# Kernel tuning notes

Measured on AMD Instinct MI355X. Metric: run time of the kernel, lower is better.

Reference implementation:

```python
import jax, jax.numpy as jnp
import numpy as np

S, E, H, D, F = 2048, 1280, 16, 80, 5120
EPS = 1e-6


def _ln(x, g, b):
    m = x.mean(-1, keepdims=True)
    v = x.var(-1, keepdims=True)
    return (x - m) * jax.lax.rsqrt(v + EPS) * g + b


def _rotate_half(x):
    x1, x2 = jnp.split(x, 2, axis=-1)
    return jnp.concatenate([-x2, x1], axis=-1)


def _quick_gelu(x):
    return x * jax.nn.sigmoid(1.702 * x)


def setup_inputs() -> dict:
    key = jax.random.key(0)
    ks = jax.random.split(key, 12)
    inp = {
        "hidden_states": jax.random.normal(ks[0], (S, E), jnp.float32),
        "attention_mask": jnp.ones((1, 1, S, S), jnp.bool_),
        "cos": jax.random.uniform(ks[1], (S, D), jnp.float32),
        "sin": jax.random.uniform(ks[2], (S, D), jnp.float32),
        "ln1_g": jnp.ones((E,), jnp.float32),
        "ln1_b": jnp.zeros((E,), jnp.float32),
        "ln2_g": jnp.ones((E,), jnp.float32),
        "ln2_b": jnp.zeros((E,), jnp.float32),
        "w_qkv": jax.random.normal(ks[3], (E, 3 * E), jnp.float32) * (E ** -0.5),
        "b_qkv": jax.random.normal(ks[4], (3 * E,), jnp.float32) * 0.02,
        "w_o": jax.random.normal(ks[5], (E, E), jnp.float32) * (E ** -0.5),
        "b_o": jax.random.normal(ks[6], (E,), jnp.float32) * 0.02,
        "w_fc1": jax.random.normal(ks[7], (E, F), jnp.float32) * (E ** -0.5),
        "b_fc1": jax.random.normal(ks[8], (F,), jnp.float32) * 0.02,
        "w_fc2": jax.random.normal(ks[9], (F, E), jnp.float32) * (F ** -0.5),
        "b_fc2": jax.random.normal(ks[10], (E,), jnp.float32) * 0.02,
    }
    return inp


def reference(hidden_states, attention_mask, cos, sin, ln1_g, ln1_b, ln2_g, ln2_b,
              w_qkv, b_qkv, w_o, b_o, w_fc1, b_fc1, w_fc2, b_fc2):
    x = hidden_states  # [S, E]
    h = _ln(x, ln1_g, ln1_b)
    qkv = h @ w_qkv + b_qkv  # [S, 3E]
    q, k, v = jnp.split(qkv, 3, axis=-1)
    q = q.reshape(S, H, D)
    k = k.reshape(S, H, D)
    v = v.reshape(S, H, D)
    # rotary in fp32, cos/sin broadcast over head axis: [S, 1, D]
    c = cos[:, None, :].astype(jnp.float32)
    s = sin[:, None, :].astype(jnp.float32)
    qf, kf = q.astype(jnp.float32), k.astype(jnp.float32)
    q = (qf * c + _rotate_half(qf) * s).astype(q.dtype)
    k = (kf * c + _rotate_half(kf) * s).astype(k.dtype)
    # attention scores [H, S, S]
    scores = jnp.einsum('shd,thd->hst', q, k) / np.float32(np.sqrt(D))
    scores = jnp.where(attention_mask[0], scores, jnp.finfo(scores.dtype).min)
    probs = jax.nn.softmax(scores.astype(jnp.float32), axis=-1).astype(q.dtype)
    attn = jnp.einsum('hst,thd->shd', probs, v).reshape(S, E)
    attn = attn @ w_o + b_o
    x = x + attn
    h2 = _ln(x, ln2_g, ln2_b)
    mlp = _quick_gelu(h2 @ w_fc1 + b_fc1) @ w_fc2 + b_fc2
    return x + mlp
```

## Files before the change

### kernel.cpp

```cpp
#include <hip/hip_runtime.h>
#include <stdint.h>
#include <math.h>

#define S_LEN 2048
#define EMB   1280
#define NHEAD 16
#define HDIM  80
#define FDIM  5120

typedef __bf16 bf16x8 __attribute__((ext_vector_type(8)));
typedef float  f32x4  __attribute__((ext_vector_type(4)));
typedef int    i32x4  __attribute__((ext_vector_type(4)));
typedef unsigned short u16x8 __attribute__((ext_vector_type(8)));
typedef unsigned short u16x4 __attribute__((ext_vector_type(4)));

__device__ __forceinline__ float b2f(unsigned short u) {
    union { float f; unsigned int i; } x; x.i = ((unsigned int)u) << 16; return x.f;
}
__device__ __forceinline__ unsigned short f2b(float f) {
    union { float f; unsigned int i; } x; x.f = f;
    unsigned int r = x.i + 0x7FFFu + ((x.i >> 16) & 1u);
    return (unsigned short)(r >> 16);
}

__device__ __forceinline__ float wave_rsum(float v) {
    #pragma unroll
    for (int o = 32; o; o >>= 1) v += __shfl_down(v, o);
    return v;
}

__device__ __forceinline__ void trans64(
    const float* __restrict__ in, unsigned short* __restrict__ out,
    int R, int C, int bx, int by, int tid)
{
    __shared__ unsigned short tile[64][65];
    int c0 = bx * 64, r0 = by * 64;
    int tx = tid & 63, ty = tid >> 6;
    #pragma unroll
    for (int j = 0; j < 16; ++j) {
        int row = ty + j * 4;
        tile[row][tx] = f2b(in[(size_t)(r0 + row) * C + c0 + tx]);
    }
    __syncthreads();
    #pragma unroll
    for (int j = 0; j < 16; ++j) {
        int row = ty + j * 4;
        out[(size_t)(c0 + row) * R + r0 + tx] = tile[tx][row];
    }
}

__global__ __launch_bounds__(256) void transpose4_kernel(
    const float* __restrict__ w_qkv, unsigned short* __restrict__ wT_qkv,
    const float* __restrict__ w_o,   unsigned short* __restrict__ wT_o,
    const float* __restrict__ w_fc1, unsigned short* __restrict__ wT_fc1,
    const float* __restrict__ w_fc2, unsigned short* __restrict__ wT_fc2)
{
    int id = blockIdx.x, tid = threadIdx.x;
    if (id < 1200) {
        trans64(w_qkv, wT_qkv, 1280, 3840, id % 60, id / 60, tid);
    } else if (id < 1600) {
        int t = id - 1200;
        trans64(w_o, wT_o, 1280, 1280, t % 20, t / 20, tid);
    } else if (id < 3200) {
        int t = id - 1600;
        trans64(w_fc1, wT_fc1, 1280, 5120, t % 80, t / 80, tid);
    } else {
        int t = id - 3200;
        trans64(w_fc2, wT_fc2, 5120, 1280, t % 20, t / 20, tid);
    }
}

__global__ __launch_bounds__(256) void ln_kernel(
    const float* __restrict__ x,
    const float* __restrict__ g,
    const float* __restrict__ b,
    unsigned short* __restrict__ out)
{
    int row = blockIdx.x, tid = threadIdx.x;
    int lane = tid & 63, wave = tid >> 6;
    const float* xr = x + (size_t)row * EMB;
    float v[5], s = 0.f, ss = 0.f;
    #pragma unroll
    for (int i = 0; i < 5; ++i) {
        float f = xr[tid + i * 256];
        v[i] = f; s += f; ss += f * f;
    }
    s = wave_rsum(s); ss = wave_rsum(ss);
    __shared__ float rs[4], rss[4];
    if (lane == 0) { rs[wave] = s; rss[wave] = ss; }
    __syncthreads();
    float st  = rs[0] + rs[1] + rs[2] + rs[3];
    float sst = rss[0] + rss[1] + rss[2] + rss[3];
    float mean = st * (1.0f / EMB);
    float var  = sst * (1.0f / EMB) - mean * mean;
    float inv  = rsqrtf(var + 1e-6f);
    unsigned short* orow = out + (size_t)row * EMB;
    #pragma unroll
    for (int i = 0; i < 5; ++i) {
        int c = tid + i * 256;
        orow[c] = f2b((v[i] - mean) * inv * g[c] + b[c]);
    }
}

template<int EPI, int OM, int SPLIT>
__global__ __launch_bounds__(256) void gemm_kernel(
    const unsigned short* __restrict__ A,
    const unsigned short* __restrict__ Bt,
    const float* __restrict__ bias,
    const float* __restrict__ res,
    void* __restrict__ Cv,
    int M, int N, int K)
{
    __shared__ __align__(16) unsigned short As[2][128 * 32];
    __shared__ __align__(16) unsigned short Bs[2][128 * 32];

    int tid = threadIdx.x;
    int lane = tid & 63, wave = tid >> 6;
    int m0 = blockIdx.x * 128, n0 = blockIdx.y * 128;
    int wm = (wave >> 1) * 64, wn = (wave & 1) * 64;
    int kc = K / SPLIT;
    int kbeg = blockIdx.z * kc;
    const int NITER = kc / 32;

    f32x4 acc[4][4];
    #pragma unroll
    for (int i = 0; i < 4; ++i)
        #pragma unroll
        for (int j = 0; j < 4; ++j)
            acc[i][j] = (f32x4){0.f, 0.f, 0.f, 0.f};

    const unsigned short* Ap0 = A  + (size_t)(m0 + (tid >> 2)) * K + (tid & 3) * 8 + kbeg;
    const unsigned short* Ap1 = Ap0 + (size_t)64 * K;
    const unsigned short* Bp0 = Bt + (size_t)(n0 + (tid >> 2)) * K + (tid & 3) * 8 + kbeg;
    const unsigned short* Bp1 = Bp0 + (size_t)64 * K;

    int arow = lane & 15, aq = (lane >> 4) * 8;
    int aoff[4], boff[4];
    #pragma unroll
    for (int i = 0; i < 4; ++i) {
        aoff[i] = (wm + i * 16 + arow) * 32 + aq;
        boff[i] = (wn + i * 16 + arow) * 32 + aq;
    }

    i32x4 rA0a, rA1a, rB0a, rB1a, rA0b, rA1b, rB0b, rB1b;

    rA0b = *(const i32x4*)(Ap0);
    rA1b = *(const i32x4*)(Ap1);
    rB0b = *(const i32x4*)(Bp0);
    rB1b = *(const i32x4*)(Bp1);
    *(i32x4*)&As[0][tid * 8]        = rA0b;
    *(i32x4*)&As[0][2048 + tid * 8] = rA1b;
    *(i32x4*)&Bs[0][tid * 8]        = rB0b;
    *(i32x4*)&Bs[0][2048 + tid * 8] = rB1b;
    if (NITER > 1) {
        rA0a = *(const i32x4*)(Ap0 + 32);
        rA1a = *(const i32x4*)(Ap1 + 32);
        rB0a = *(const i32x4*)(Bp0 + 32);
        rB1a = *(const i32x4*)(Bp1 + 32);
    }
    __syncthreads();

#define GSTEP(IT, AW0, AW1, BW0, BW1, AL0, AL1, BL0, BL1)                    \
    {                                                                         \
        const int cur = (IT) & 1, nb = cur ^ 1;                               \
        if ((IT) + 1 < NITER) {                                               \
            *(i32x4*)&As[nb][tid * 8]        = AW0;                           \
            *(i32x4*)&As[nb][2048 + tid * 8] = AW1;                           \
            *(i32x4*)&Bs[nb][tid * 8]        = BW0;                           \
            *(i32x4*)&Bs[nb][2048 + tid * 8] = BW1;                           \
        }                                                                     \
        if ((IT) + 2 < NITER) {                                               \
            int ko = ((IT) + 2) * 32;                                         \
            AL0 = *(const i32x4*)(Ap0 + ko);                                  \
            AL1 = *(const i32x4*)(Ap1 + ko);                                  \
            BL0 = *(const i32x4*)(Bp0 + ko);                                  \
            BL1 = *(const i32x4*)(Bp1 + ko);                                  \
        }                                                                     \
        bf16x8 af[4], bfm[4];                                                 \
        _Pragma("unroll") for (int i = 0; i < 4; ++i) {                       \
            af[i]  = *(const bf16x8*)&As[cur][aoff[i]];                       \
            bfm[i] = *(const bf16x8*)&Bs[cur][boff[i]];                       \
        }                                                                     \
        _Pragma("unroll") for (int mi = 0; mi < 4; ++mi)                      \
            _Pragma("unroll") for (int ni = 0; ni < 4; ++ni)                  \
                acc[mi][ni] = __builtin_amdgcn_mfma_f32_16x16x32_bf16(        \
                    af[mi], bfm[ni], acc[mi][ni], 0, 0, 0);                   \
        __syncthreads();                                                      \
    }

    for (int it = 0; it < NITER; it += 2) {
        GSTEP(it,     rA0a, rA1a, rB0a, rB1a, rA0b, rA1b, rB0b, rB1b)
        GSTEP(it + 1, rA0b, rA1b, rB0b, rB1b, rA0a, rA1a, rB0a, rB1a)
    }
#undef GSTEP

    int col = lane & 15;
    int rbase = (lane >> 4) * 4;
    #pragma unroll
    for (int ni = 0; ni < 4; ++ni) {
        int gn = n0 + wn + ni * 16 + col;
        float bv = (OM == 2) ? 0.f : bias[gn];
        #pragma unroll
        for (int mi = 0; mi < 4; ++mi) {
            int gm = m0 + wm + mi * 16 + rbase;
            #pragma unroll
            for (int r = 0; r < 4; ++r) {
                float v = acc[mi][ni][r] + bv;
                if (OM != 2) {
                    if (EPI == 1) v = v / (1.0f + expf(-1.702f * v));
                }
                if (OM == 2)
                    ((float*)Cv)[((size_t)blockIdx.z * M + gm + r) * N + gn] = v;
                else if (OM == 1)
                    ((float*)Cv)[(size_t)(gm + r) * N + gn] = v;
                else
                    ((unsigned short*)Cv)[(size_t)(gm + r) * N + gn] = f2b(v);
            }
        }
    }
}

template<int Z>
__global__ __launch_bounds__(256) void reduceZ_kernel(
    const float* __restrict__ part,
    const float* __restrict__ res,
    const float* __restrict__ bias,
    float* __restrict__ out)
{
    size_t i4 = ((size_t)blockIdx.x * 256 + threadIdx.x) * 4;
    int colb = (int)(i4 % EMB);
    f32x4 a = *(const f32x4*)&res[i4];
    f32x4 bv = *(const f32x4*)&bias[colb];
    a += bv;
    const size_t slice = (size_t)S_LEN * EMB;
    #pragma unroll
    for (int z = 0; z < Z; ++z)
        a += *(const f32x4*)&part[z * slice + i4];
    *(f32x4*)&out[i4] = a;
}

__global__ __launch_bounds__(256) void ropev_kernel(
    const unsigned short* __restrict__ qkv,
    const float* __restrict__ cosb,
    const float* __restrict__ sinb,
    unsigned short* __restrict__ q_out,
    unsigned short* __restrict__ k_out,
    unsigned short* __restrict__ vt)
{
    __shared__ unsigned short qT[64 * 84];
    __shared__ unsigned short kT[64 * 84];
    __shared__ unsigned short vT[64 * 84];

    int h = blockIdx.x >> 5, stile = blockIdx.x & 31;
    int s0 = stile * 64;
    int tid = threadIdx.x;

    u16x4 qr[5], kr[5];
    #pragma unroll
    for (int i = 0; i < 5; ++i) {
        int u = tid + i * 256;
        int row = u / 20, col = (u % 20) * 4;
        const unsigned short* base = qkv + (size_t)(s0 + row) * (3 * EMB) + h * HDIM + col;
        qr[i] = *(const u16x4*)base;
        kr[i] = *(const u16x4*)(base + EMB);
        u16x4 v4 = *(const u16x4*)(base + 2 * EMB);
        *(u16x4*)&qT[row * 84 + col] = qr[i];
        *(u16x4*)&kT[row * 84 + col] = kr[i];
        *(u16x4*)&vT[row * 84 + col] = v4;
    }
    __syncthreads();

    #pragma unroll
    for (int i = 0; i < 5; ++i) {
        int u = tid + i * 256;
        int row = u / 20, col = (u % 20) * 4;
        int pcol = (col < 40) ? col + 40 : col - 40;
        float sgn = (col < 40) ? -1.f : 1.f;
        u16x4 qp = *(const u16x4*)&qT[row * 84 + pcol];
        u16x4 kp = *(const u16x4*)&kT[row * 84 + pcol];
        f32x4 c4 = *(const f32x4*)&cosb[(size_t)(s0 + row) * HDIM + col];
        f32x4 s4 = *(const f32x4*)&sinb[(size_t)(s0 + row) * HDIM + col];
        u16x4 qo, ko;
        #pragma unroll
        for (int j = 0; j < 4; ++j) {
            qo[j] = f2b(b2f(qr[i][j]) * c4[j] + sgn * b2f(qp[j]) * s4[j]);
            ko[j] = f2b(b2f(kr[i][j]) * c4[j] + sgn * b2f(kp[j]) * s4[j]);
        }
        size_t o = ((size_t)h * S_LEN + s0 + row) * HDIM + col;
        *(u16x4*)&q_out[o] = qo;
        *(u16x4*)&k_out[o] = ko;
    }
    #pragma unroll
    for (int i = 0; i < 5; ++i) {
        int w = tid + i * 256;
        int d = w >> 4, c4i = (w & 15) * 4;
        u16x4 pk;
        #pragma unroll
        for (int j = 0; j < 4; ++j) pk[j] = vT[(c4i + j) * 84 + d];
        *(u16x4*)(vt + ((size_t)h * HDIM + d) * S_LEN + s0 + c4i) = pk;
    }
}

__global__ __launch_bounds__(256) void fattn_kernel(
    const unsigned short* __restrict__ q,
    const unsigned short* __restrict__ k,
    const unsigned short* __restrict__ vt,
    unsigned short* __restrict__ out)
{
    __shared__ __align__(16) unsigned short Ks[2][64 * 96];
    __shared__ __align__(16) unsigned short Vs[2][80 * 72];
    __shared__ __align__(16) unsigned short Pt[4 * 16 * 72];

    int tid = threadIdx.x;
    int lane = tid & 63, wave = tid >> 6;
    int arow = lane & 15, quad = lane >> 4;
    int h = blockIdx.x >> 5, qb = blockIdx.x & 31;
    int s0 = qb * 64;
    const float c = 0.16129856f;

    const unsigned short* kbase = k + (size_t)h * S_LEN * HDIM;
    const unsigned short* vbase = vt + (size_t)h * HDIM * S_LEN;

    bf16x8 qf[3];
    {
        const unsigned short* qrp =
            q + ((size_t)h * S_LEN + s0 + wave * 16 + arow) * HDIM;
        #pragma unroll
        for (int kk = 0; kk < 3; ++kk) {
            int col = kk * 32 + quad * 8;
            u16x8 qv = (u16x8){0, 0, 0, 0, 0, 0, 0, 0};
            if (col < HDIM) qv = *(const u16x8*)(qrp + col);
            u16x8 qs8;
            #pragma unroll
            for (int j = 0; j < 8; ++j) qs8[j] = f2b(b2f(qv[j]) * c);
            qf[kk] = *(bf16x8*)&qs8;
        }
    }

    {
        int zr = tid >> 2, zc = 80 + (tid & 3) * 4;
        int zidx = (zr * 96 + zc) ^ ((zr & 7) << 3);
        *(u16x4*)&Ks[0][zidx] = (u16x4){0, 0, 0, 0};
        *(u16x4*)&Ks[1][zidx] = (u16x4){0, 0, 0, 0};
    }

    u16x4 kreg[5], vreg[5];
    #pragma unroll
    for (int i = 0; i < 5; ++i) {
        int u = tid + i * 256;
        kreg[i] = *(const u16x4*)(kbase + u * 4);
        vreg[i] = *(const u16x4*)(vbase + (size_t)(u >> 4) * S_LEN + (u & 15) * 4);
    }
    #pragma unroll
    for (int i = 0; i < 5; ++i) {
        int u = tid + i * 256;
        int row = u / 20, c4 = (u % 20) * 4;
        *(u16x4*)&Ks[0][(row * 96 + c4) ^ ((row & 7) << 3)] = kreg[i];
        *(u16x4*)&Vs[0][(u >> 4) * 72 + (u & 15) * 4] = vreg[i];
    }
    #pragma unroll
    for (int i = 0; i < 5; ++i) {
        int u = tid + i * 256;
        kreg[i] = *(const u16x4*)(kbase + (size_t)64 * HDIM + u * 4);
        vreg[i] = *(const u16x4*)(vbase + (size_t)(u >> 4) * S_LEN + 64 + (u & 15) * 4);
    }
    __syncthreads();

    int ksw[3];
    #pragma unroll
    for (int kk = 0; kk < 3; ++kk)
        ksw[kk] = (arow * 96 + kk * 32 + quad * 8) ^ ((arow & 7) << 3);

    int pw = wave * 16 * 72;
    float l_part = 0.f;
    f32x4 o[5];
    #pragma unroll
    for (int di = 0; di < 5; ++di) o[di] = (f32x4){0.f, 0.f, 0.f, 0.f};

    const int NIT = S_LEN / 64;
    for (int it = 0; it < NIT; ++it) {
        int cur = it & 1;
        if (it + 1 < NIT) {
            int nb = (it + 1) & 1;
            #pragma unroll
            for (int i = 0; i < 5; ++i) {
                int u = tid + i * 256;
                int row = u / 20, c4 = (u % 20) * 4;
                *(u16x4*)&Ks[nb][(row * 96 + c4) ^ ((row & 7) << 3)] = kreg[i];
                *(u16x4*)&Vs[nb][(u >> 4) * 72 + (u & 15) * 4] = vreg[i];
            }
        }
        if (it + 2 < NIT) {
            int t0 = (it + 2) * 64;
            #pragma unroll
            for (int i = 0; i < 5; ++i) {
                int u = tid + i * 256;
                kreg[i] = *(const u16x4*)(kbase + (size_t)t0 * HDIM + u * 4);
                vreg[i] = *(const u16x4*)(vbase + (size_t)(u >> 4) * S_LEN + t0 + (u & 15) * 4);
            }
        }

        f32x4 sc[4];
        #pragma unroll
        for (int ni = 0; ni < 4; ++ni) sc[ni] = (f32x4){0.f, 0.f, 0.f, 0.f};
        __builtin_amdgcn_s_setprio(1);
        #pragma unroll
        for (int kk = 0; kk < 3; ++kk) {
            bf16x8 bq = qf[kk];
            #pragma unroll
            for (int ni = 0; ni < 4; ++ni) {
                bf16x8 ak = *(const bf16x8*)&Ks[cur][ksw[kk] + ni * 1536];
                sc[ni] = __builtin_amdgcn_mfma_f32_16x16x32_bf16(ak, bq, sc[ni], 0, 0, 0);
            }
        }
        __builtin_amdgcn_s_setprio(0);

        #pragma unroll
        for (int ni = 0; ni < 4; ++ni) {
            u16x4 pk;
            #pragma unroll
            for (int r = 0; r < 4; ++r) {
                float p = __builtin_amdgcn_exp2f(sc[ni][r]);
                l_part += p;
                __bf16 pb = (__bf16)p;
                pk[r] = *(unsigned short*)&pb;
            }
            *(u16x4*)&Pt[pw + arow * 72 + ni * 16 + quad * 4] = pk;
        }

        __builtin_amdgcn_s_setprio(1);
        #pragma unroll
        for (int kk = 0; kk < 2; ++kk) {
            bf16x8 ap = *(const bf16x8*)&Pt[pw + arow * 72 + kk * 32 + quad * 8];
            #pragma unroll
            for (int di = 0; di < 5; ++di) {
                bf16x8 bv = *(const bf16x8*)&Vs[cur][(di * 16 + arow) * 72 + kk * 32 + quad * 8];
                o[di] = __builtin_amdgcn_mfma_f32_16x16x32_bf16(ap, bv, o[di], 0, 0, 0);
            }
        }
        __builtin_amdgcn_s_setprio(0);

        __syncthreads();
    }

    float l_run = l_part;
    l_run += __shfl_xor(l_run, 16);
    l_run += __shfl_xor(l_run, 32);

    float inv[4];
    #pragma unroll
    for (int r = 0; r < 4; ++r)
        inv[r] = 1.f / __shfl(l_run, (lane & 48) | (quad * 4 + r));
    #pragma unroll
    for (int r = 0; r < 4; ++r) {
        int gq = s0 + wave * 16 + quad * 4 + r;
        unsigned short* op = out + (size_t)gq * EMB + h * HDIM;
        #pragma unroll
        for (int di = 0; di < 5; ++di)
            op[di * 16 + arow] = f2b(o[di][r] * inv[r]);
    }
}

extern "C" void kernel_launch(void* const* d_in, const int* in_sizes, int n_in,
                              void* d_out, int out_size, void* d_ws, size_t ws_size,
                              hipStream_t stream)
{
    const float* hidden = (const float*)d_in[0];
    const float* cosb  = (const float*)d_in[2];
    const float* sinb  = (const float*)d_in[3];
    const float* ln1g  = (const float*)d_in[4];
    const float* ln1b  = (const float*)d_in[5];
    const float* ln2g  = (const float*)d_in[6];
    const float* ln2b  = (const float*)d_in[7];
    const float* w_qkv = (const float*)d_in[8];
    const float* b_qkv = (const float*)d_in[9];
    const float* w_o   = (const float*)d_in[10];
    const float* b_o   = (const float*)d_in[11];
    const float* w_fc1 = (const float*)d_in[12];
    const float* b_fc1 = (const float*)d_in[13];
    const float* w_fc2 = (const float*)d_in[14];
    const float* b_fc2 = (const float*)d_in[15];

    char* ws = (char*)d_ws;
    size_t off = 0;
    auto alloc = [&](size_t bytes) -> void* {
        void* p = (void*)(ws + off);
        off += (bytes + 255) & ~(size_t)255;
        return p;
    };
    unsigned short* wT_qkv = (unsigned short*)alloc((size_t)3840 * 1280 * 2);
    unsigned short* wT_o   = (unsigned short*)alloc((size_t)1280 * 1280 * 2);
    unsigned short* wT_fc1 = (unsigned short*)alloc((size_t)5120 * 1280 * 2);
    unsigned short* wT_fc2 = (unsigned short*)alloc((size_t)1280 * 5120 * 2);
    unsigned short* h1     = (unsigned short*)alloc((size_t)S_LEN * EMB * 2);
    unsigned short* qkv    = (unsigned short*)alloc((size_t)S_LEN * 3 * EMB * 2);
    unsigned short* q_r    = (unsigned short*)alloc((size_t)S_LEN * EMB * 2);
    unsigned short* k_r    = (unsigned short*)alloc((size_t)S_LEN * EMB * 2);
    unsigned short* vt_g   = (unsigned short*)alloc((size_t)S_LEN * EMB * 2);
    unsigned short* attn_o = (unsigned short*)alloc((size_t)S_LEN * EMB * 2);
    float*          x1     = (float*)alloc((size_t)S_LEN * EMB * 4);
    unsigned short* h2     = (unsigned short*)alloc((size_t)S_LEN * EMB * 2);
    unsigned short* mlp1   = (unsigned short*)alloc((size_t)S_LEN * FDIM * 2);
    float* partials = (float*)h1;

    transpose4_kernel<<<4800, 256, 0, stream>>>(
        w_qkv, wT_qkv, w_o, wT_o, w_fc1, wT_fc1, w_fc2, wT_fc2);

    ln_kernel<<<S_LEN, 256, 0, stream>>>(hidden, ln1g, ln1b, h1);

    gemm_kernel<0, 0, 1><<<dim3(S_LEN / 128, 3840 / 128, 1), 256, 0, stream>>>(
        h1, wT_qkv, b_qkv, nullptr, qkv, S_LEN, 3 * EMB, EMB);

    ropev_kernel<<<NHEAD * (S_LEN / 64), 256, 0, stream>>>(qkv, cosb, sinb, q_r, k_r, vt_g);

    fattn_kernel<<<NHEAD * (S_LEN / 64), 256, 0, stream>>>(q_r, k_r, vt_g, attn_o);

    gemm_kernel<0, 2, 2><<<dim3(S_LEN / 128, 1280 / 128, 2), 256, 0, stream>>>(
        attn_o, wT_o, b_o, nullptr, partials, S_LEN, EMB, EMB);
    reduceZ_kernel<2><<<(S_LEN * EMB / 4) / 256, 256, 0, stream>>>(
        partials, hidden, b_o, x1);

    ln_kernel<<<S_LEN, 256, 0, stream>>>(x1, ln2g, ln2b, h2);

    gemm_kernel<1, 0, 1><<<dim3(S_LEN / 128, FDIM / 128, 1), 256, 0, stream>>>(
        h2, wT_fc1, b_fc1, nullptr, mlp1, S_LEN, FDIM, EMB);

    gemm_kernel<0, 2, 4><<<dim3(S_LEN / 128, 1280 / 128, 4), 256, 0, stream>>>(
        mlp1, wT_fc2, b_fc2, nullptr, partials, S_LEN, EMB, FDIM);
    reduceZ_kernel<4><<<(S_LEN * EMB / 4) / 256, 256, 0, stream>>>(
        partials, x1, b_fc2, (float*)d_out);
}
```

Baseline: 362.7 us.

## Use atomic split-K accumulation, XCD-aware block remap, and LDS swizzles

```diff
diff --git a/kernel.cpp b/kernel.cpp
--- a/kernel.cpp
+++ b/kernel.cpp
@@ -102,12 +102,22 @@
     }
 }
 
+__global__ __launch_bounds__(256) void addbias_kernel(
+    const float* __restrict__ res,
+    const float* __restrict__ bias,
+    float* __restrict__ out)
+{
+    size_t i4 = ((size_t)blockIdx.x * 256 + threadIdx.x) * 4;
+    f32x4 a = *(const f32x4*)&res[i4];
+    f32x4 bv = *(const f32x4*)&bias[(int)(i4 % EMB)];
+    *(f32x4*)&out[i4] = a + bv;
+}
+
 template<int EPI, int OM, int SPLIT>
 __global__ __launch_bounds__(256) void gemm_kernel(
     const unsigned short* __restrict__ A,
     const unsigned short* __restrict__ Bt,
     const float* __restrict__ bias,
-    const float* __restrict__ res,
     void* __restrict__ Cv,
     int M, int N, int K)
 {
@@ -116,10 +126,21 @@
 
     int tid = threadIdx.x;
     int lane = tid & 63, wave = tid >> 6;
-    int m0 = blockIdx.x * 128, n0 = blockIdx.y * 128;
+
+    int gx = gridDim.x, gy = gridDim.y;
+    int nwg = gx * gy * gridDim.z;
+    int flat = blockIdx.x + gx * (blockIdx.y + gy * blockIdx.z);
+    int cpx = nwg >> 3;
+    int logical = (flat & 7) * cpx + (flat >> 3);
+    int bx = logical % gx;
+    int rem = logical / gx;
+    int by = rem % gy;
+    int bz = rem / gy;
+
+    int m0 = bx * 128, n0 = by * 128;
     int wm = (wave >> 1) * 64, wn = (wave & 1) * 64;
     int kc = K / SPLIT;
-    int kbeg = blockIdx.z * kc;
+    int kbeg = bz * kc;
     const int NITER = kc / 32;
 
     f32x4 acc[4][4];
@@ -129,17 +150,19 @@
         for (int j = 0; j < 4; ++j)
             acc[i][j] = (f32x4){0.f, 0.f, 0.f, 0.f};
 
-    const unsigned short* Ap0 = A  + (size_t)(m0 + (tid >> 2)) * K + (tid & 3) * 8 + kbeg;
+    int u = tid ^ ((tid >> 3) & 7);
+    const unsigned short* Ap0 = A  + (size_t)(m0 + (u >> 2)) * K + (u & 3) * 8 + kbeg;
     const unsigned short* Ap1 = Ap0 + (size_t)64 * K;
-    const unsigned short* Bp0 = Bt + (size_t)(n0 + (tid >> 2)) * K + (tid & 3) * 8 + kbeg;
+    const unsigned short* Bp0 = Bt + (size_t)(n0 + (u >> 2)) * K + (u & 3) * 8 + kbeg;
     const unsigned short* Bp1 = Bp0 + (size_t)64 * K;
 
     int arow = lane & 15, aq = (lane >> 4) * 8;
+    int aswz = ((arow >> 1) & 7) << 3;
     int aoff[4], boff[4];
     #pragma unroll
     for (int i = 0; i < 4; ++i) {
-        aoff[i] = (wm + i * 16 + arow) * 32 + aq;
-        boff[i] = (wn + i * 16 + arow) * 32 + aq;
+        aoff[i] = ((wm + i * 16 + arow) * 32 + aq) ^ aswz;
+        boff[i] = ((wn + i * 16 + arow) * 32 + aq) ^ aswz;
     }
 
     i32x4 rA0a, rA1a, rB0a, rB1a, rA0b, rA1b, rB0b, rB1b;
@@ -199,18 +222,18 @@
     #pragma unroll
     for (int ni = 0; ni < 4; ++ni) {
         int gn = n0 + wn + ni * 16 + col;
-        float bv = (OM == 2) ? 0.f : bias[gn];
+        float bv = (OM == 3) ? 0.f : bias[gn];
         #pragma unroll
         for (int mi = 0; mi < 4; ++mi) {
             int gm = m0 + wm + mi * 16 + rbase;
             #pragma unroll
             for (int r = 0; r < 4; ++r) {
                 float v = acc[mi][ni][r] + bv;
-                if (OM != 2) {
+                if (OM != 3) {
                     if (EPI == 1) v = v / (1.0f + expf(-1.702f * v));
                 }
-                if (OM == 2)
-                    ((float*)Cv)[((size_t)blockIdx.z * M + gm + r) * N + gn] = v;
+                if (OM == 3)
+                    atomicAdd(&((float*)Cv)[(size_t)(gm + r) * N + gn], v);
                 else if (OM == 1)
                     ((float*)Cv)[(size_t)(gm + r) * N + gn] = v;
                 else
@@ -218,25 +241,6 @@
             }
         }
     }
-}
-
-template<int Z>
-__global__ __launch_bounds__(256) void reduceZ_kernel(
-    const float* __restrict__ part,
-    const float* __restrict__ res,
-    const float* __restrict__ bias,
-    float* __restrict__ out)
-{
-    size_t i4 = ((size_t)blockIdx.x * 256 + threadIdx.x) * 4;
-    int colb = (int)(i4 % EMB);
-    f32x4 a = *(const f32x4*)&res[i4];
-    f32x4 bv = *(const f32x4*)&bias[colb];
-    a += bv;
-    const size_t slice = (size_t)S_LEN * EMB;
-    #pragma unroll
-    for (int z = 0; z < Z; ++z)
-        a += *(const f32x4*)&part[z * slice + i4];
-    *(f32x4*)&out[i4] = a;
 }
 
 __global__ __launch_bounds__(256) void ropev_kernel(
@@ -314,7 +318,8 @@
     int tid = threadIdx.x;
     int lane = tid & 63, wave = tid >> 6;
     int arow = lane & 15, quad = lane >> 4;
-    int h = blockIdx.x >> 5, qb = blockIdx.x & 31;
+    int logical = (blockIdx.x & 7) * 64 + (blockIdx.x >> 3);
+    int h = logical >> 5, qb = logical & 31;
     int s0 = qb * 64;
     const float c = 0.16129856f;
 
@@ -372,6 +377,8 @@
         ksw[kk] = (arow * 96 + kk * 32 + quad * 8) ^ ((arow & 7) << 3);
 
     int pw = wave * 16 * 72;
+    int poff = pw + arow * 72 + ((arow >> 3) << 2);
+
     float l_part = 0.f;
     f32x4 o[5];
     #pragma unroll
@@ -425,13 +432,17 @@
                 __bf16 pb = (__bf16)p;
                 pk[r] = *(unsigned short*)&pb;
             }
-            *(u16x4*)&Pt[pw + arow * 72 + ni * 16 + quad * 4] = pk;
+            *(u16x4*)&Pt[poff + ni * 16 + quad * 4] = pk;
         }
 
         __builtin_amdgcn_s_setprio(1);
         #pragma unroll
         for (int kk = 0; kk < 2; ++kk) {
-            bf16x8 ap = *(const bf16x8*)&Pt[pw + arow * 72 + kk * 32 + quad * 8];
+            u16x4 plo = *(const u16x4*)&Pt[poff + kk * 32 + quad * 8];
+            u16x4 phi = *(const u16x4*)&Pt[poff + kk * 32 + quad * 8 + 4];
+            u16x8 apu = (u16x8){plo[0], plo[1], plo[2], plo[3],
+                                phi[0], phi[1], phi[2], phi[3]};
+            bf16x8 ap = *(bf16x8*)&apu;
             #pragma unroll
             for (int di = 0; di < 5; ++di) {
                 bf16x8 bv = *(const bf16x8*)&Vs[cur][(di * 16 + arow) * 72 + kk * 32 + quad * 8];
@@ -501,7 +512,6 @@
     float*          x1     = (float*)alloc((size_t)S_LEN * EMB * 4);
     unsigned short* h2     = (unsigned short*)alloc((size_t)S_LEN * EMB * 2);
     unsigned short* mlp1   = (unsigned short*)alloc((size_t)S_LEN * FDIM * 2);
-    float* partials = (float*)h1;
 
     transpose4_kernel<<<4800, 256, 0, stream>>>(
         w_qkv, wT_qkv, w_o, wT_o, w_fc1, wT_fc1, w_fc2, wT_fc2);
@@ -509,24 +519,22 @@
     ln_kernel<<<S_LEN, 256, 0, stream>>>(hidden, ln1g, ln1b, h1);
 
     gemm_kernel<0, 0, 1><<<dim3(S_LEN / 128, 3840 / 128, 1), 256, 0, stream>>>(
-        h1, wT_qkv, b_qkv, nullptr, qkv, S_LEN, 3 * EMB, EMB);
+        h1, wT_qkv, b_qkv, qkv, S_LEN, 3 * EMB, EMB);
 
     ropev_kernel<<<NHEAD * (S_LEN / 64), 256, 0, stream>>>(qkv, cosb, sinb, q_r, k_r, vt_g);
 
     fattn_kernel<<<NHEAD * (S_LEN / 64), 256, 0, stream>>>(q_r, k_r, vt_g, attn_o);
 
-    gemm_kernel<0, 2, 2><<<dim3(S_LEN / 128, 1280 / 128, 2), 256, 0, stream>>>(
-        attn_o, wT_o, b_o, nullptr, partials, S_LEN, EMB, EMB);
-    reduceZ_kernel<2><<<(S_LEN * EMB / 4) / 256, 256, 0, stream>>>(
-        partials, hidden, b_o, x1);
+    addbias_kernel<<<(S_LEN * EMB / 4) / 256, 256, 0, stream>>>(hidden, b_o, x1);
+    gemm_kernel<0, 3, 2><<<dim3(S_LEN / 128, 1280 / 128, 2), 256, 0, stream>>>(
+        attn_o, wT_o, nullptr, x1, S_LEN, EMB, EMB);
 
     ln_kernel<<<S_LEN, 256, 0, stream>>>(x1, ln2g, ln2b, h2);
 
     gemm_kernel<1, 0, 1><<<dim3(S_LEN / 128, FDIM / 128, 1), 256, 0, stream>>>(
-        h2, wT_fc1, b_fc1, nullptr, mlp1, S_LEN, FDIM, EMB);
-
-    gemm_kernel<0, 2, 4><<<dim3(S_LEN / 128, 1280 / 128, 4), 256, 0, stream>>>(
-        mlp1, wT_fc2, b_fc2, nullptr, partials, S_LEN, EMB, FDIM);
-    reduceZ_kernel<4><<<(S_LEN * EMB / 4) / 256, 256, 0, stream>>>(
-        partials, x1, b_fc2, (float*)d_out);
-}
+        h2, wT_fc1, b_fc1, mlp1, S_LEN, FDIM, EMB);
+
+    addbias_kernel<<<(S_LEN * EMB / 4) / 256, 256, 0, stream>>>(x1, b_fc2, (float*)d_out);
+    gemm_kernel<0, 3, 4><<<dim3(S_LEN / 128, 1280 / 128, 4), 256, 0, stream>>>(
+        mlp1, wT_fc2, nullptr, (float*)d_out, S_LEN, EMB, FDIM);
+}
```

New measurement: 378.8 us. 4.4% more time.
